# Kernel optimization log

Hardware: AMD Instinct MI355X
Metric: run time of the kernel (lower is better)

The kernel has to match this reference:

```python
import jax, jax.numpy as jnp
import numpy as np
from jax import lax

B, Hm, Wm, C, HEADS, MLP_H = 16, 56, 56, 256, 4, 1024
N = Hm * Wm
GRID_STRIDE = 4
N_GRID = (Hm // GRID_STRIDE) * (Wm // GRID_STRIDE)  # 196
K_DOWN = N // 4                                      # 784
K_ADA = K_DOWN - N_GRID
H2, W2 = Hm // 2, Wm // 2
POOL = 7


def _token_order():
    # get_loc: grid tokens first, then adaptive tokens
    pos = np.arange(N)
    tmp = pos.reshape(Hm, Wm)
    pos_grid = tmp[GRID_STRIDE // 2::GRID_STRIDE, GRID_STRIDE // 2::GRID_STRIDE].reshape(-1)
    m = np.ones(N, bool)
    m[pos_grid] = False
    return np.concatenate([pos_grid, pos[m]])


def _loc_init():
    y = 2.0 * ((np.arange(Hm) + 0.5) / Hm) - 1.0
    x = 2.0 * ((np.arange(Wm) + 0.5) / Wm) - 1.0
    xm, ym = np.meshgrid(x, y)
    return np.stack([xm, ym], -1).reshape(-1, 2).astype(np.float32)


_ORDER = _token_order()
_LOC = _loc_init()[_ORDER]


def _ln(x, g, b, eps=1e-5):
    m = jnp.mean(x, -1, keepdims=True)
    v = jnp.mean((x - m) ** 2, -1, keepdims=True)
    return (x - m) * lax.rsqrt(v + eps) * g + b


def _gauss_kernel(ks=3, sigma=2.0):
    c = np.arange(ks, dtype=np.float32)
    xg = np.tile(c, ks).reshape(ks, ks)
    yg = xg.T
    mean = (ks - 1) / 2.0
    var = sigma ** 2
    k = np.exp(-((xg - mean) ** 2 + (yg - mean) ** 2) / (2 * var)) / (2 * np.pi * var)
    return (k / k.sum()).astype(np.float32)


def _gauss_filt(x):
    ch = x.shape[1]
    w = jnp.broadcast_to(jnp.asarray(_gauss_kernel())[None, None], (ch, 1, 3, 3))
    return lax.conv_general_dilated(x, w, (1, 1), [(1, 1), (1, 1)],
                                    feature_group_count=ch,
                                    dimension_numbers=('NCHW', 'OIHW', 'NCHW'))


def _token2map(x, loc, H, W):
    # scatter-add tokens into a [H,W] map, average by count, gaussian hole-fill
    b, n, c = x.shape
    loc = jnp.clip(loc, -1, 1)
    px = jnp.clip(jnp.round(0.5 * (loc[..., 0] + 1) * W - 0.5).astype(jnp.int32), 0, W - 1)
    py = jnp.clip(jnp.round(0.5 * (loc[..., 1] + 1) * H - 0.5).astype(jnp.int32), 0, H - 1)
    idx = (px + py * W + jnp.arange(b)[:, None] * H * W).reshape(-1)
    src = jnp.concatenate([x, jnp.ones((b, n, 1), x.dtype)], -1).reshape(b * n, c + 1)
    out = jnp.zeros((b * H * W, c + 1), x.dtype).at[idx].add(src)
    out = out.reshape(b, H, W, c + 1).transpose(0, 3, 1, 2)
    feat, mask = out[:, :c], out[:, c:]
    feat = feat / (mask + 1e-6)
    mask = (mask > 0).astype(x.dtype)
    feat = feat * mask
    # reconstruct_feature (kernel_size=3, sigma=2)
    fm = _gauss_filt(jnp.concatenate([feat, mask], 1))
    fi = fm[:, :c] / (fm[:, c:] + 1e-6)
    mi = (fm[:, c:] > 0).astype(x.dtype)
    fi = fi * mi
    return feat + (1 - mask) * fi


def _map2token(fm, loc):
    # bilinear grid_sample, align_corners=False, zeros padding
    b, c, H, W = fm.shape
    x = (loc[..., 0] + 1) * 0.5 * W - 0.5
    y = (loc[..., 1] + 1) * 0.5 * H - 0.5
    x0 = jnp.floor(x)
    y0 = jnp.floor(y)
    wx = x - x0
    wy = y - y0
    fm_flat = fm.reshape(b, c, H * W)

    def gather(xi, yi):
        valid = ((xi >= 0) & (xi < W) & (yi >= 0) & (yi < H)).astype(fm.dtype)
        ii = (jnp.clip(yi, 0, H - 1) * W + jnp.clip(xi, 0, W - 1)).astype(jnp.int32)
        v = jnp.take_along_axis(fm_flat, ii[:, None, :], axis=2)  # [b,c,k]
        return v * valid[:, None, :]

    x0i = x0.astype(jnp.int32)
    y0i = y0.astype(jnp.int32)
    v00 = gather(x0i, y0i)
    v01 = gather(x0i + 1, y0i)
    v10 = gather(x0i, y0i + 1)
    v11 = gather(x0i + 1, y0i + 1)
    wx = wx[:, None, :]
    wy = wy[:, None, :]
    out = (v00 * (1 - wx) * (1 - wy) + v01 * wx * (1 - wy)
           + v10 * (1 - wx) * wy + v11 * wx * wy)
    return out.transpose(0, 2, 1)  # [b,k,c]


def _forward(x, ln1_g, ln1_b, wq, wkv, wproj, bproj, sr_w, sr_b, srn_g, srn_b,
             ln2_g, ln2_b, fc1_w, fc1_b, dw_w, dw_b, fc2_w, fc2_b, conf_w, conf_b):
    order = jnp.asarray(_ORDER)
    x = jnp.take(x, order, axis=1)                       # get_loc reorder
    loc = jnp.broadcast_to(jnp.asarray(_LOC)[None], (B, N, 2))
    d = C // HEADS
    # ---- PVT attention (spatial-reduction via 7x7 adaptive pool + 1x1 conv)
    xn = _ln(x, ln1_g, ln1_b)
    q = (xn @ wq).reshape(B, N, HEADS, d).transpose(0, 2, 1, 3)
    fmap = xn.transpose(0, 2, 1).reshape(B, C, Hm, Wm)
    pooled = fmap.reshape(B, C, POOL, Hm // POOL, POOL, Wm // POOL).mean((3, 5))
    sr = jnp.einsum('bihw,oi->bohw', pooled, sr_w) + sr_b[None, :, None, None]
    t = sr.reshape(B, C, POOL * POOL).transpose(0, 2, 1)
    t = jax.nn.gelu(_ln(t, srn_g, srn_b), approximate=False)
    kv = (t @ wkv).reshape(B, POOL * POOL, 2, HEADS, d)
    k = kv[:, :, 0].transpose(0, 2, 1, 3)
    v = kv[:, :, 1].transpose(0, 2, 1, 3)
    a = jax.nn.softmax(jnp.einsum('bhnd,bhmd->bhnm', q, k) * (d ** -0.5), axis=-1)
    o = jnp.einsum('bhnm,bhmd->bhnd', a, v).transpose(0, 2, 1, 3).reshape(B, N, C)
    x = x + o @ wproj + bproj
    # ---- MLP with depthwise conv
    xn = _ln(x, ln2_g, ln2_b)
    h = jax.nn.relu(xn @ fc1_w + fc1_b)
    hm = h.transpose(0, 2, 1).reshape(B, MLP_H, Hm, Wm)
    hm = lax.conv_general_dilated(hm, dw_w, (1, 1), [(1, 1), (1, 1)],
                                  feature_group_count=MLP_H,
                                  dimension_numbers=('NCHW', 'OIHW', 'NCHW'))
    hm = hm + dw_b[None, :, None, None]
    h = jax.nn.gelu(hm.reshape(B, MLP_H, N).transpose(0, 2, 1), approximate=False)
    x = x + h @ fc2_w + fc2_b
    # ---- gumbel top-k selection among adaptive tokens (grid tokens kept)
    conf = (x @ conf_w + conf_b)[..., 0]                 # [B,N]
    u = jax.random.uniform(jax.random.key(1), (B, N - N_GRID), x.dtype)
    g = -jnp.log(-jnp.log(u + 1e-6) + 1e-6)
    scores = conf[:, N_GRID:] + g                        # T=1
    _, idx = lax.top_k(scores, K_ADA)
    x_ada = jnp.take_along_axis(x[:, N_GRID:], idx[..., None], axis=1)
    loc_ada = jnp.take_along_axis(loc[:, N_GRID:], idx[..., None], axis=1)
    x_down = jnp.concatenate([x[:, :N_GRID], x_ada], 1)      # [B,784,C]
    loc_down = jnp.concatenate([loc[:, :N_GRID], loc_ada], 1)
    # ---- token2map (scatter-add + gaussian fill) then map2token (grid sample)
    fmap2 = _token2map(x, loc, H2, W2)
    tok = _map2token(fmap2, loc_down)
    return x_down + tok


def setup_inputs() -> dict:
    key = jax.random.key(0)
    ks = jax.random.split(key, 10)
    s = 0.02

    def rn(k, shape):
        return jax.random.normal(k, shape, jnp.float32) * s

    return {
        'x': jax.random.normal(ks[0], (B, N, C), jnp.float32),
        'ln1_g': jnp.ones((C,), jnp.float32), 'ln1_b': jnp.zeros((C,), jnp.float32),
        'wq': rn(ks[1], (C, C)), 'wkv': rn(ks[2], (C, 2 * C)),
        'wproj': rn(ks[3], (C, C)), 'bproj': jnp.zeros((C,), jnp.float32),
        'sr_w': rn(ks[4], (C, C)), 'sr_b': jnp.zeros((C,), jnp.float32),
        'srn_g': jnp.ones((C,), jnp.float32), 'srn_b': jnp.zeros((C,), jnp.float32),
        'ln2_g': jnp.ones((C,), jnp.float32), 'ln2_b': jnp.zeros((C,), jnp.float32),
        'fc1_w': rn(ks[5], (C, MLP_H)), 'fc1_b': jnp.zeros((MLP_H,), jnp.float32),
        'dw_w': rn(ks[6], (MLP_H, 1, 3, 3)), 'dw_b': jnp.zeros((MLP_H,), jnp.float32),
        'fc2_w': rn(ks[7], (MLP_H, C)), 'fc2_b': jnp.zeros((C,), jnp.float32),
        'conf_w': rn(ks[8], (C, 1)), 'conf_b': jnp.zeros((1,), jnp.float32),
    }


def reference(x, ln1_g, ln1_b, wq, wkv, wproj, bproj, sr_w, sr_b, srn_g, srn_b,
              ln2_g, ln2_b, fc1_w, fc1_b, dw_w, dw_b, fc2_w, fc2_b, conf_w, conf_b):
    return _forward(x, ln1_g, ln1_b, wq, wkv, wproj, bproj, sr_w, sr_b, srn_g, srn_b,
                    ln2_g, ln2_b, fc1_w, fc1_b, dw_w, dw_b, fc2_w, fc2_b, conf_w, conf_b)
```

## Files before the change

kernel.cpp:

```cpp
#include <hip/hip_runtime.h>
#include <math.h>


#define BB 16
#define NN 3136
#define CC 256
#define NHEADS 4
#define DH 64
#define MLPH 1024
#define NGRID 196
#define NREST 2940
#define KADA 588
#define HW 56
#define BCH 2

__device__ __forceinline__ int inv_order(int p) {
  int r = p / HW, c = p % HW;
  if ((r & 3) == 2 && (c & 3) == 2) return (r >> 2) * 14 + (c >> 2);
  int g = ((r + 1) >> 2) * 14 + (((r & 3) == 2) ? ((c + 1) >> 2) : 0);
  return NGRID + p - g;
}

__device__ __forceinline__ double gelu_d(double v) {
  return 0.5 * v * (1.0 + erf(v * 0.70710678118654752440));
}

__device__ __forceinline__ void tf2x32k(unsigned k0, unsigned k1, unsigned x0, unsigned x1,
                                        unsigned& o0, unsigned& o1) {
  unsigned ks[3] = {k0, k1, k0 ^ k1 ^ 0x1BD11BDAu};
  x0 += ks[0]; x1 += ks[1];
  const int rot[2][4] = {{13,15,26,6},{17,29,16,24}};
  #pragma unroll
  for (int i = 0; i < 5; ++i) {
    #pragma unroll
    for (int j = 0; j < 4; ++j) {
      int rr = rot[i & 1][j];
      x0 += x1;
      x1 = (x1 << rr) | (x1 >> (32 - rr));
      x1 ^= x0;
    }
    x0 += ks[(i + 1) % 3];
    x1 += ks[(i + 2) % 3] + (unsigned)(i + 1);
  }
  o0 = x0; o1 = x1;
}

__device__ bool tf_kat() {
  unsigned a, b;
  tf2x32k(0u, 0u, 0u, 0u, a, b);
  if (a != 0x6b200159u || b != 0x99ba4efeu) return false;
  tf2x32k(0xffffffffu, 0xffffffffu, 0xffffffffu, 0xffffffffu, a, b);
  if (a != 0x1cb996fcu || b != 0xbb002be7u) return false;
  tf2x32k(0x13198a2eu, 0x03707344u, 0x243f6a88u, 0x85a308d3u, a, b);
  if (a != 0xc4923a9cu || b != 0x483df7a0u) return false;
  return true;
}

__device__ __forceinline__ double gumbel_d(int f) {
  unsigned o0, o1;
  tf2x32k(0u, 1u, 0u, (unsigned)f, o0, o1);
  unsigned bits = o0 ^ o1;
  float u = __uint_as_float((bits >> 9) | 0x3f800000u) - 1.0f;
  double ud = (double)u;
  return -log(-log(ud + 1e-6) + 1e-6);
}

__global__ void k_order(int* __restrict__ ord) {
  int p = blockIdx.x * 256 + threadIdx.x;
  if (p < NN) ord[inv_order(p)] = p;
}

__global__ __launch_bounds__(256) void k_ln1(const float* __restrict__ x,
    const float* __restrict__ g, const float* __restrict__ b2,
    float* __restrict__ x_r, float* __restrict__ xn) {
  int b = blockIdx.x / NN, p = blockIdx.x % NN;
  int t = threadIdx.x;
  __shared__ double la[4], lb[4];
  float v = x[((size_t)b*NN + p)*CC + t];
  double vd = (double)v;
  double s = vd;
  #pragma unroll
  for (int o = 32; o; o >>= 1) s += __shfl_xor(s, o, 64);
  if ((t & 63) == 0) la[t >> 6] = s;
  __syncthreads();
  double m = (la[0] + la[1] + la[2] + la[3]) * (1.0/CC);
  double d = vd - m;
  s = d * d;
  #pragma unroll
  for (int o = 32; o; o >>= 1) s += __shfl_xor(s, o, 64);
  if ((t & 63) == 0) lb[t >> 6] = s;
  __syncthreads();
  double var = (lb[0] + lb[1] + lb[2] + lb[3]) * (1.0/CC);
  double o2 = d * (1.0 / sqrt(var + 1e-5)) * (double)g[t] + (double)b2[t];
  int n = inv_order(p);
  size_t dst = ((size_t)b*NN + n)*CC + t;
  x_r[dst] = v;
  xn[dst] = (float)o2;
}

__global__ __launch_bounds__(256) void k_ln2(const float* __restrict__ xin,
    const float* __restrict__ g, const float* __restrict__ b2, float* __restrict__ xo) {
  int row = blockIdx.x;
  int t = threadIdx.x;
  __shared__ double la[4], lb[4];
  double v = (double)xin[(size_t)row*CC + t];
  double s = v;
  #pragma unroll
  for (int o = 32; o; o >>= 1) s += __shfl_xor(s, o, 64);
  if ((t & 63) == 0) la[t >> 6] = s;
  __syncthreads();
  double m = (la[0] + la[1] + la[2] + la[3]) * (1.0/CC);
  double d = v - m;
  s = d * d;
  #pragma unroll
  for (int o = 32; o; o >>= 1) s += __shfl_xor(s, o, 64);
  if ((t & 63) == 0) lb[t >> 6] = s;
  __syncthreads();
  double var = (lb[0] + lb[1] + lb[2] + lb[3]) * (1.0/CC);
  xo[(size_t)row*CC + t] = (float)(d * (1.0 / sqrt(var + 1e-5)) * (double)g[t] + (double)b2[t]);
}

__global__ __launch_bounds__(256) void k_sr(const float* __restrict__ xn,
    const float* __restrict__ sr_w, const float* __restrict__ sr_b, float* __restrict__ srout) {
  int b = blockIdx.x / 49, cell = blockIdx.x % 49;
  int p1 = cell / 7, p2 = cell % 7;
  int t = threadIdx.x;
  __shared__ double pl[256];
  double s = 0.0;
  #pragma unroll
  for (int i = 0; i < 8; ++i)
    #pragma unroll
    for (int j = 0; j < 8; ++j) {
      int n = (p1*8 + i)*HW + (p2*8 + j);
      s += (double)xn[((size_t)b*NN + n)*CC + t];
    }
  pl[t] = s * (1.0/64.0);
  __syncthreads();
  double acc = (double)sr_b[t];
  for (int i = 0; i < CC; ++i) acc += pl[i] * (double)sr_w[t*CC + i];
  srout[((size_t)b*49 + cell)*CC + t] = (float)acc;
}

__global__ __launch_bounds__(256) void k_kv(const float* __restrict__ srout,
    const float* __restrict__ g, const float* __restrict__ b2,
    const float* __restrict__ wkv, float* __restrict__ kb, float* __restrict__ vb) {
  int b = blockIdx.x / 49, m = blockIdx.x % 49;
  int t = threadIdx.x;
  __shared__ double la[4], lb[4];
  __shared__ double tl[256];
  double v = (double)srout[((size_t)b*49 + m)*CC + t];
  double s = v;
  #pragma unroll
  for (int o = 32; o; o >>= 1) s += __shfl_xor(s, o, 64);
  if ((t & 63) == 0) la[t >> 6] = s;
  __syncthreads();
  double mean = (la[0] + la[1] + la[2] + la[3]) * (1.0/CC);
  double d = v - mean;
  s = d * d;
  #pragma unroll
  for (int o = 32; o; o >>= 1) s += __shfl_xor(s, o, 64);
  if ((t & 63) == 0) lb[t >> 6] = s;
  __syncthreads();
  double var = (lb[0] + lb[1] + lb[2] + lb[3]) * (1.0/CC);
  double o2 = d * (1.0 / sqrt(var + 1e-5)) * (double)g[t] + (double)b2[t];
  tl[t] = gelu_d(o2);
  __syncthreads();
  #pragma unroll
  for (int rep = 0; rep < 2; ++rep) {
    int j = t + rep*256;
    double acc = 0.0;
    for (int i = 0; i < CC; ++i) acc += tl[i] * (double)wkv[(size_t)i*512 + j];
    int h = (j >> 6) & 3, dd = j & 63;
    float* dst = (j >> 8) ? vb : kb;
    dst[(((size_t)b*NHEADS + h)*49 + m)*DH + dd] = (float)acc;
  }
}

template<int BIAS, int RELU, int RESID>
__global__ __launch_bounds__(256, 2) void k_gemmC(const float* __restrict__ A,
    const float* __restrict__ Bw, const float* __restrict__ bias,
    const float* resid, float* Co, int M, int N, int K) {
  __shared__ __align__(16) float As[16][132];
  __shared__ __align__(16) float Bs[16][132];
  int tid = threadIdx.x;
  int n0 = blockIdx.x * 128, m0 = blockIdx.y * 128;
  int tx = tid & 15, ty = tid >> 4;
  int aM = tid >> 1, aK = (tid & 1) * 8;
  int bK = tid >> 4, bN = (tid & 15) * 8;
  double acc[8][8] = {};
  for (int k0 = 0; k0 < K; k0 += 16) {
    const float* Ap = A + (size_t)(m0 + aM) * K + k0 + aK;
    float4 a0 = *(const float4*)Ap;
    float4 a1 = *(const float4*)(Ap + 4);
    As[aK+0][aM] = a0.x; As[aK+1][aM] = a0.y; As[aK+2][aM] = a0.z; As[aK+3][aM] = a0.w;
    As[aK+4][aM] = a1.x; As[aK+5][aM] = a1.y; As[aK+6][aM] = a1.z; As[aK+7][aM] = a1.w;
    const float* Bp = Bw + (size_t)(k0 + bK) * N + n0 + bN;
    *(float4*)&Bs[bK][bN]     = *(const float4*)Bp;
    *(float4*)&Bs[bK][bN + 4] = *(const float4*)(Bp + 4);
    __syncthreads();
    #pragma unroll
    for (int k = 0; k < 16; ++k) {
      double av[8], bv[8];
      #pragma unroll
      for (int r = 0; r < 8; ++r) av[r] = (double)As[k][ty*8 + r];
      #pragma unroll
      for (int c = 0; c < 8; ++c) bv[c] = (double)Bs[k][tx*8 + c];
      #pragma unroll
      for (int r = 0; r < 8; ++r)
        #pragma unroll
        for (int c = 0; c < 8; ++c)
          acc[r][c] = fma(av[r], bv[c], acc[r][c]);
    }
    __syncthreads();
  }
  #pragma unroll
  for (int r = 0; r < 8; ++r) {
    size_t off = (size_t)(m0 + ty*8 + r) * N + n0 + tx*8;
    #pragma unroll
    for (int c = 0; c < 8; ++c) {
      double v = acc[r][c];
      if (BIAS)  v += (double)bias[n0 + tx*8 + c];
      if (RESID) v += (double)resid[off + c];
      if (RELU)  v = fmax(v, 0.0);
      Co[off + c] = (float)v;
    }
  }
}

template<int BIAS, int RELU, int RESID>
__global__ __launch_bounds__(256) void k_gemmA(const float* __restrict__ A,
    const float* __restrict__ Bw, const float* __restrict__ bias,
    const float* resid, float* Co, int M, int N, int K) {
  __shared__ __align__(16) float As[16][132];
  __shared__ __align__(16) float Bs[16][68];
  int tid = threadIdx.x;
  int n0 = blockIdx.x * 64, m0 = blockIdx.y * 128;
  int tx = tid & 15, ty = tid >> 4;
  int aM = tid >> 2, aK = (tid & 3) * 4;
  int bK = tid >> 4, bN = (tid & 15) * 4;
  double acc[8][4] = {};
  for (int k0 = 0; k0 < K; k0 += 16) {
    #pragma unroll
    for (int ps = 0; ps < 2; ++ps) {
      float4 a4 = *(const float4*)&A[(size_t)(m0 + aM + ps*64) * K + k0 + aK];
      As[aK+0][aM+ps*64] = a4.x; As[aK+1][aM+ps*64] = a4.y;
      As[aK+2][aM+ps*64] = a4.z; As[aK+3][aM+ps*64] = a4.w;
    }
    float4 b4 = *(const float4*)&Bw[(size_t)(k0 + bK) * N + n0 + bN];
    *(float4*)&Bs[bK][bN] = b4;
    __syncthreads();
    #pragma unroll
    for (int k = 0; k < 16; ++k) {
      double av[8], bv[4];
      #pragma unroll
      for (int r = 0; r < 8; ++r) av[r] = (double)As[k][ty*8 + r];
      #pragma unroll
      for (int c = 0; c < 4; ++c) bv[c] = (double)Bs[k][tx*4 + c];
      #pragma unroll
      for (int r = 0; r < 8; ++r)
        #pragma unroll
        for (int c = 0; c < 4; ++c)
          acc[r][c] = fma(av[r], bv[c], acc[r][c]);
    }
    __syncthreads();
  }
  #pragma unroll
  for (int r = 0; r < 8; ++r) {
    size_t off = (size_t)(m0 + ty*8 + r) * N + n0 + tx*4;
    #pragma unroll
    for (int c = 0; c < 4; ++c) {
      double v = acc[r][c];
      if (BIAS)  v += (double)bias[n0 + tx*4 + c];
      if (RESID) v += (double)resid[off + c];
      if (RELU)  v = fmax(v, 0.0);
      Co[off + c] = (float)v;
    }
  }
}

__global__ __launch_bounds__(256) void k_attn(float* __restrict__ q,
    const float* __restrict__ kb, const float* __restrict__ vb) {
  int bh = blockIdx.x / 49, tile = blockIdx.x % 49;
  int b = bh >> 2, h = bh & 3;
  int tid = threadIdx.x;
  int w = tid >> 6, lane = tid & 63;
  __shared__ float Kt[64][53];
  __shared__ float Vs[49][64];
  __shared__ float qsw[4][64];
  __shared__ double Ps[4][52];
  const size_t kvbase = ((size_t)bh * 49) * DH;
  for (int idx = tid; idx < 49*64; idx += 256) {
    int m = idx >> 6, d = idx & 63;
    Kt[d][m] = kb[kvbase + idx];
    ((float*)Vs)[idx] = vb[kvbase + idx];
  }
  __syncthreads();
  #pragma unroll 1
  for (int t16 = 0; t16 < 16; ++t16) {
    int tok = tile*64 + w*16 + t16;
    size_t qoff = ((size_t)b*NN + tok)*CC + h*64 + lane;
    qsw[w][lane] = q[qoff];
    double lg = -1e300;
    if (lane < 49) {
      double acc = 0.0;
      #pragma unroll 16
      for (int d = 0; d < 64; ++d)
        acc = fma((double)qsw[w][d], (double)Kt[d][lane], acc);
      lg = acc * 0.125;
    }
    double mx = lg;
    #pragma unroll
    for (int o = 32; o; o >>= 1) mx = fmax(mx, __shfl_xor(mx, o, 64));
    double e = (lane < 49) ? exp(lg - mx) : 0.0;
    double s = e;
    #pragma unroll
    for (int o = 32; o; o >>= 1) s += __shfl_xor(s, o, 64);
    double sinv = 1.0 / s;
    if (lane < 49) Ps[w][lane] = e;
    double acc = 0.0;
    #pragma unroll 7
    for (int m = 0; m < 49; ++m)
      acc = fma(Ps[w][m], (double)Vs[m][lane], acc);
    q[qoff] = (float)(acc * sinv);
  }
}

__global__ __launch_bounds__(256) void k_dw(const float* __restrict__ hb,
    const float* __restrict__ w, const float* __restrict__ bias, float* __restrict__ h2) {
  int bl = blockIdx.x / NN, n = blockIdx.x % NN;
  int r = n / HW, c = n % HW;
  int t = threadIdx.x;
  const size_t base = (size_t)bl * NN;
  #pragma unroll
  for (int it = 0; it < 4; ++it) {
    int mc = t + it*256;
    double acc = (double)bias[mc];
    #pragma unroll
    for (int ky = 0; ky < 3; ++ky) {
      int rr = r + ky - 1;
      if (rr < 0 || rr >= HW) continue;
      #pragma unroll
      for (int kx = 0; kx < 3; ++kx) {
        int cc2 = c + kx - 1;
        if (cc2 < 0 || cc2 >= HW) continue;
        acc = fma((double)w[mc*9 + ky*3 + kx], (double)hb[(base + rr*HW + cc2)*MLPH + mc], acc);
      }
    }
    h2[(base + n)*MLPH + mc] = (float)gelu_d(acc);
  }
}

__global__ __launch_bounds__(256) void k_conf(const float* __restrict__ x3,
    const float* __restrict__ cw, const float* __restrict__ cb, double* __restrict__ scd) {
  int wid = (blockIdx.x * 256 + threadIdx.x) >> 6;
  int lane = threadIdx.x & 63;
  if (wid >= BB * NREST) return;
  int b = wid / NREST, i = wid % NREST;
  const float* xr = x3 + ((size_t)b*NN + NGRID + i)*CC;
  double acc = 0.0;
  #pragma unroll
  for (int r = 0; r < 4; ++r)
    acc += (double)xr[lane + r*64] * (double)cw[lane + r*64];
  #pragma unroll
  for (int o = 32; o; o >>= 1) acc += __shfl_xor(acc, o, 64);
  if (lane == 0) scd[wid] = acc + (double)cb[0] + gumbel_d(wid);
}

__global__ __launch_bounds__(512) void k_topk2(const double* __restrict__ scd, int* __restrict__ sel) {
  int b = blockIdx.x / 6, chunk = blockIdx.x % 6;
  __shared__ double sc[NREST];
  const double* s = scd + (size_t)b * NREST;
  for (int j = threadIdx.x; j < NREST; j += 512) sc[j] = s[j];
  __syncthreads();
  int i = chunk * 512 + threadIdx.x;
  if (i < NREST) {
    double si = sc[i];
    int rank = 0;
    #pragma unroll 8
    for (int j = 0; j < NREST; ++j) {
      double sj = sc[j];
      rank += (int)((sj > si) | ((sj == si) & (j < i)));
    }
    if (rank < KADA) sel[b*KADA + rank] = NGRID + i;
  }
}

__global__ __launch_bounds__(256) void k_t2m(const float* __restrict__ x3, float* __restrict__ fm) {
  int b = blockIdx.x / 784, pix = blockIdx.x % 784;
  int py = pix / 28, px = pix % 28;
  int t = threadIdx.x;
  float s = 0.f;
  #pragma unroll
  for (int dy = 0; dy < 2; ++dy)
    #pragma unroll
    for (int dx = 0; dx < 2; ++dx) {
      int p = (2*py + dy)*HW + 2*px + dx;
      s += x3[((size_t)b*NN + inv_order(p))*CC + t];
    }
  fm[((size_t)b*784 + pix)*CC + t] = s * (1.0f / 4.000001f);
}

__global__ __launch_bounds__(256) void k_out(const float* __restrict__ x3,
    const float* __restrict__ fm, const int* __restrict__ sel,
    const int* __restrict__ ord, float* __restrict__ out) {
  int b = blockIdx.x / 784, slot = blockIdx.x % 784;
  int t = threadIdx.x;
  int n = (slot < NGRID) ? slot : sel[b*KADA + slot - NGRID];
  int p = ord[n];
  int r = p / HW, c = p % HW;
  int ix0 = (c - 1) >> 1;
  int iy0 = (r - 1) >> 1;
  float wx = (c & 1) ? 0.25f : 0.75f;
  float wy = (r & 1) ? 0.25f : 0.75f;
  const float* fb = fm + (size_t)b*784*CC + t;
  float v = 0.f;
  float w00 = (1.f-wx)*(1.f-wy), w01 = wx*(1.f-wy), w10 = (1.f-wx)*wy, w11 = wx*wy;
  if (ix0 >= 0   && iy0 >= 0)   v += w00 * fb[(iy0*28 + ix0)*CC];
  if (ix0+1 < 28 && iy0 >= 0)   v += w01 * fb[(iy0*28 + ix0+1)*CC];
  if (ix0 >= 0   && iy0+1 < 28) v += w10 * fb[((iy0+1)*28 + ix0)*CC];
  if (ix0+1 < 28 && iy0+1 < 28) v += w11 * fb[((iy0+1)*28 + ix0+1)*CC];
  float res = x3[((size_t)b*NN + n)*CC + t] + v;
  if (blockIdx.x == 0 && t == 0) {
    if (!tf_kat()) res += 1000.0f;
  }
  out[((size_t)b*784 + slot)*CC + t] = res;
}

extern "C" void kernel_launch(void* const* d_in, const int* in_sizes, int n_in,
                              void* d_out, int out_size, void* d_ws, size_t ws_size,
                              hipStream_t stream) {
  const float* x      = (const float*)d_in[0];
  const float* ln1_g  = (const float*)d_in[1];
  const float* ln1_b  = (const float*)d_in[2];
  const float* wq     = (const float*)d_in[3];
  const float* wkv    = (const float*)d_in[4];
  const float* wproj  = (const float*)d_in[5];
  const float* bproj  = (const float*)d_in[6];
  const float* sr_w   = (const float*)d_in[7];
  const float* sr_b   = (const float*)d_in[8];
  const float* srn_g  = (const float*)d_in[9];
  const float* srn_b  = (const float*)d_in[10];
  const float* ln2_g  = (const float*)d_in[11];
  const float* ln2_b  = (const float*)d_in[12];
  const float* fc1_w  = (const float*)d_in[13];
  const float* fc1_b  = (const float*)d_in[14];
  const float* dw_w   = (const float*)d_in[15];
  const float* dw_b   = (const float*)d_in[16];
  const float* fc2_w  = (const float*)d_in[17];
  const float* fc2_b  = (const float*)d_in[18];
  const float* conf_w = (const float*)d_in[19];
  const float* conf_b = (const float*)d_in[20];
  float* out = (float*)d_out;

  float* ws = (float*)d_ws;
  const size_t SZ_XN = (size_t)BB*NN*CC;
  const size_t SZ_H  = (size_t)BCH*NN*MLPH;
  float* x_r   = ws;
  float* xn    = x_r + SZ_XN;
  float* qbuf  = xn + SZ_XN;
  float* hb    = qbuf + SZ_XN;
  float* h2b   = hb + SZ_H;
  float* srout = h2b + SZ_H;
  float* kb    = srout + (size_t)BB*49*CC;
  float* vb    = kb + (size_t)BB*NHEADS*49*DH;
  float* fm    = vb + (size_t)BB*NHEADS*49*DH;
  double* scd  = (double*)(fm + (size_t)BB*784*CC);
  int*   sel   = (int*)(scd + (size_t)BB*NREST);
  int*   ord   = sel + BB*KADA;

  k_order<<<(NN+255)/256, 256, 0, stream>>>(ord);
  k_ln1<<<BB*NN, 256, 0, stream>>>(x, ln1_g, ln1_b, x_r, xn);
  k_sr<<<BB*49, 256, 0, stream>>>(xn, sr_w, sr_b, srout);
  k_kv<<<BB*49, 256, 0, stream>>>(srout, srn_g, srn_b, wkv, kb, vb);
  k_gemmC<0,0,0><<<dim3(CC/128, BB*NN/128), 256, 0, stream>>>(xn, wq, nullptr, nullptr, qbuf, BB*NN, CC, CC);
  k_attn<<<BB*NHEADS*49, 256, 0, stream>>>(qbuf, kb, vb);
  k_gemmC<1,0,1><<<dim3(CC/128, BB*NN/128), 256, 0, stream>>>(qbuf, wproj, bproj, x_r, x_r, BB*NN, CC, CC);
  k_ln2<<<BB*NN, 256, 0, stream>>>(x_r, ln2_g, ln2_b, xn);
  for (int bc = 0; bc < BB/BCH; ++bc) {
    const size_t ro = (size_t)bc * BCH * NN;
    k_gemmC<1,1,0><<<dim3(MLPH/128, BCH*NN/128), 256, 0, stream>>>(xn + ro*CC, fc1_w, fc1_b, nullptr, hb, BCH*NN, MLPH, CC);
    k_dw<<<BCH*NN, 256, 0, stream>>>(hb, dw_w, dw_b, h2b);
    k_gemmA<1,0,1><<<dim3(CC/64, BCH*NN/128), 256, 0, stream>>>(h2b, fc2_w, fc2_b, x_r + ro*CC, x_r + ro*CC, BCH*NN, CC, MLPH);
  }
  k_conf<<<(BB*NREST*64 + 255)/256, 256, 0, stream>>>(x_r, conf_w, conf_b, scd);
  k_topk2<<<BB*6, 512, 0, stream>>>(scd, sel);
  k_t2m<<<BB*784, 256, 0, stream>>>(x_r, fm);
  k_out<<<BB*784, 256, 0, stream>>>(x_r, fm, sel, ord, out);
}
```

Measured before the change: 3.733 ms.

## Use FP64 MFMA matrix instructions for all dense GEMMs with runtime layout probe

Replaces the scalar double-precision FMA GEMM kernels (gemmC and gemmA) with one kernel built on the 16x16x4 f64 MFMA instruction. Each wave computes a 64x64 sub-tile. A tiny probe kernel runs first and finds the operand and output lane layout at runtime, and the GEMM reads that layout to index its operands and write back. The aim is to move the FP64 matrix work from vector ALUs to matrix cores; the cost is an extra launch, runtime-indexed addressing, and scattered epilogue stores. The fc2 GEMM now uses 128-wide N tiles, halving its block count.

```diff
diff --git a/kernel.cpp b/kernel.cpp
--- a/kernel.cpp
+++ b/kernel.cpp
@@ -14,6 +14,8 @@
 #define HW 56
 #define BCH 2
 
+typedef double v4d __attribute__((ext_vector_type(4)));
+
 __device__ __forceinline__ int inv_order(int p) {
   int r = p / HW, c = p % HW;
   if ((r & 3) == 2 && (c & 3) == 2) return (r >> 2) * 14 + (c >> 2);
@@ -65,6 +67,42 @@
   return -log(-log(ud + 1e-6) + 1e-6);
 }
 
+__global__ __launch_bounds__(64) void k_probe(int* __restrict__ combo) {
+  int l = threadIdx.x;
+  __shared__ double Am[16][4];
+  __shared__ double Bm[4][16];
+  __shared__ int found;
+  if (l == 0) found = -1;
+  {
+    int i = l >> 2, k = l & 3;
+    Am[i][k] = (double)((i*7 + k*3) % 13) - 6.0;
+    int k2 = l >> 4, j = l & 15;
+    Bm[k2][j] = (double)((k2*5 + j*11) % 17) - 8.0;
+  }
+  __syncthreads();
+  for (int c = 0; c < 16; ++c) {
+    int asw = c & 1, bsw = (c >> 1) & 1, dtr = (c >> 2) & 1, din = (c >> 3) & 1;
+    double a = Am[asw ? (l >> 2) : (l & 15)][asw ? (l & 3) : (l >> 4)];
+    double b = Bm[bsw ? (l & 3) : (l >> 4)][bsw ? (l >> 2) : (l & 15)];
+    v4d d = (v4d){0.0, 0.0, 0.0, 0.0};
+    d = __builtin_amdgcn_mfma_f64_16x16x4f64(a, b, d, 0, 0, 0);
+    int ok = 1;
+    #pragma unroll
+    for (int r = 0; r < 4; ++r) {
+      int rl = din ? ((l >> 4) + 4*r) : ((l >> 4)*4 + r);
+      int cl = l & 15;
+      int row = dtr ? cl : rl, col = dtr ? rl : cl;
+      double ref = 0.0;
+      #pragma unroll
+      for (int k = 0; k < 4; ++k) ref += Am[row][k] * Bm[k][col];
+      ok &= (d[r] == ref) ? 1 : 0;
+    }
+    if (__all(ok) && l == 0 && found < 0) found = c;
+  }
+  __syncthreads();
+  if (l == 0) combo[0] = found;
+}
+
 __global__ void k_order(int* __restrict__ ord) {
   int p = blockIdx.x * 256 + threadIdx.x;
   if (p < NN) ord[inv_order(p)] = p;
@@ -177,17 +215,30 @@
 }
 
 template<int BIAS, int RELU, int RESID>
-__global__ __launch_bounds__(256, 2) void k_gemmC(const float* __restrict__ A,
+__global__ __launch_bounds__(256) void k_gemmM(const float* __restrict__ A,
     const float* __restrict__ Bw, const float* __restrict__ bias,
-    const float* resid, float* Co, int M, int N, int K) {
-  __shared__ __align__(16) float As[16][132];
-  __shared__ __align__(16) float Bs[16][132];
+    const float* resid, float* Co, int M, int N, int K,
+    const int* __restrict__ combo) {
+  __shared__ float As[16][136];
+  __shared__ float Bs[16][136];
+  int cc = combo[0];
+  int asw = cc & 1, bsw = (cc >> 1) & 1, dtr = (cc >> 2) & 1, din = (cc >> 3) & 1;
   int tid = threadIdx.x;
   int n0 = blockIdx.x * 128, m0 = blockIdx.y * 128;
-  int tx = tid & 15, ty = tid >> 4;
+  int w = tid >> 6, lane = tid & 63;
+  int wr = w >> 1, wc = w & 1;
+  int raA = asw ? (lane >> 2) : (lane & 15);
+  int kaA = asw ? (lane & 3)  : (lane >> 4);
+  int rbB = bsw ? (lane >> 2) : (lane & 15);
+  int kbB = bsw ? (lane & 3)  : (lane >> 4);
   int aM = tid >> 1, aK = (tid & 1) * 8;
   int bK = tid >> 4, bN = (tid & 15) * 8;
-  double acc[8][8] = {};
+  v4d acc[4][4];
+  #pragma unroll
+  for (int m = 0; m < 4; ++m)
+    #pragma unroll
+    for (int n = 0; n < 4; ++n)
+      acc[m][n] = (v4d){0.0, 0.0, 0.0, 0.0};
   for (int k0 = 0; k0 < K; k0 += 16) {
     const float* Ap = A + (size_t)(m0 + aM) * K + k0 + aK;
     float4 a0 = *(const float4*)Ap;
@@ -199,81 +250,39 @@
     *(float4*)&Bs[bK][bN + 4] = *(const float4*)(Bp + 4);
     __syncthreads();
     #pragma unroll
-    for (int k = 0; k < 16; ++k) {
-      double av[8], bv[8];
+    for (int kk = 0; kk < 4; ++kk) {
+      double af[4], bf[4];
       #pragma unroll
-      for (int r = 0; r < 8; ++r) av[r] = (double)As[k][ty*8 + r];
+      for (int m = 0; m < 4; ++m) af[m] = (double)As[kk*4 + kaA][wr*64 + m*16 + raA];
       #pragma unroll
-      for (int c = 0; c < 8; ++c) bv[c] = (double)Bs[k][tx*8 + c];
+      for (int n = 0; n < 4; ++n) bf[n] = (double)Bs[kk*4 + kbB][wc*64 + n*16 + rbB];
       #pragma unroll
-      for (int r = 0; r < 8; ++r)
+      for (int m = 0; m < 4; ++m)
         #pragma unroll
-        for (int c = 0; c < 8; ++c)
-          acc[r][c] = fma(av[r], bv[c], acc[r][c]);
+        for (int n = 0; n < 4; ++n)
+          acc[m][n] = __builtin_amdgcn_mfma_f64_16x16x4f64(af[m], bf[n], acc[m][n], 0, 0, 0);
     }
     __syncthreads();
   }
-  #pragma unroll
-  for (int r = 0; r < 8; ++r) {
-    size_t off = (size_t)(m0 + ty*8 + r) * N + n0 + tx*8;
-    #pragma unroll
-    for (int c = 0; c < 8; ++c) {
-      double v = acc[r][c];
-      if (BIAS)  v += (double)bias[n0 + tx*8 + c];
-      if (RESID) v += (double)resid[off + c];
-      if (RELU)  v = fmax(v, 0.0);
-      Co[off + c] = (float)v;
-    }
-  }
-}
-
-template<int BIAS, int RELU, int RESID>
-__global__ __launch_bounds__(256) void k_gemmA(const float* __restrict__ A,
-    const float* __restrict__ Bw, const float* __restrict__ bias,
-    const float* resid, float* Co, int M, int N, int K) {
-  __shared__ __align__(16) float As[16][132];
-  __shared__ __align__(16) float Bs[16][68];
-  int tid = threadIdx.x;
-  int n0 = blockIdx.x * 64, m0 = blockIdx.y * 128;
-  int tx = tid & 15, ty = tid >> 4;
-  int aM = tid >> 2, aK = (tid & 3) * 4;
-  int bK = tid >> 4, bN = (tid & 15) * 4;
-  double acc[8][4] = {};
-  for (int k0 = 0; k0 < K; k0 += 16) {
-    #pragma unroll
-    for (int ps = 0; ps < 2; ++ps) {
-      float4 a4 = *(const float4*)&A[(size_t)(m0 + aM + ps*64) * K + k0 + aK];
-      As[aK+0][aM+ps*64] = a4.x; As[aK+1][aM+ps*64] = a4.y;
-      As[aK+2][aM+ps*64] = a4.z; As[aK+3][aM+ps*64] = a4.w;
-    }
-    float4 b4 = *(const float4*)&Bw[(size_t)(k0 + bK) * N + n0 + bN];
-    *(float4*)&Bs[bK][bN] = b4;
-    __syncthreads();
-    #pragma unroll
-    for (int k = 0; k < 16; ++k) {
-      double av[8], bv[4];
+  int lk = lane >> 4, lr = lane & 15;
+  #pragma unroll
+  for (int m = 0; m < 4; ++m) {
+    #pragma unroll
+    for (int n = 0; n < 4; ++n) {
       #pragma unroll
-      for (int r = 0; r < 8; ++r) av[r] = (double)As[k][ty*8 + r];
-      #pragma unroll
-      for (int c = 0; c < 4; ++c) bv[c] = (double)Bs[k][tx*4 + c];
-      #pragma unroll
-      for (int r = 0; r < 8; ++r)
-        #pragma unroll
-        for (int c = 0; c < 4; ++c)
-          acc[r][c] = fma(av[r], bv[c], acc[r][c]);
-    }
-    __syncthreads();
-  }
-  #pragma unroll
-  for (int r = 0; r < 8; ++r) {
-    size_t off = (size_t)(m0 + ty*8 + r) * N + n0 + tx*4;
-    #pragma unroll
-    for (int c = 0; c < 4; ++c) {
-      double v = acc[r][c];
-      if (BIAS)  v += (double)bias[n0 + tx*4 + c];
-      if (RESID) v += (double)resid[off + c];
-      if (RELU)  v = fmax(v, 0.0);
-      Co[off + c] = (float)v;
+      for (int r = 0; r < 4; ++r) {
+        int rl = din ? (lk + 4*r) : (lk*4 + r);
+        int rloc = dtr ? lr : rl;
+        int cloc = dtr ? rl : lr;
+        int row = m0 + wr*64 + m*16 + rloc;
+        int col = n0 + wc*64 + n*16 + cloc;
+        size_t off = (size_t)row * N + col;
+        double v = acc[m][n][r];
+        if (BIAS)  v += (double)bias[col];
+        if (RESID) v += (double)resid[off];
+        if (RELU)  v = fmax(v, 0.0);
+        Co[off] = (float)v;
+      }
     }
   }
 }
@@ -402,7 +411,8 @@
 
 __global__ __launch_bounds__(256) void k_out(const float* __restrict__ x3,
     const float* __restrict__ fm, const int* __restrict__ sel,
-    const int* __restrict__ ord, float* __restrict__ out) {
+    const int* __restrict__ ord, const int* __restrict__ combo,
+    float* __restrict__ out) {
   int b = blockIdx.x / 784, slot = blockIdx.x % 784;
   int t = threadIdx.x;
   int n = (slot < NGRID) ? slot : sel[b*KADA + slot - NGRID];
@@ -422,6 +432,7 @@
   float res = x3[((size_t)b*NN + n)*CC + t] + v;
   if (blockIdx.x == 0 && t == 0) {
     if (!tf_kat()) res += 1000.0f;
+    if (combo[0] < 0) res += 2000.0f;
   }
   out[((size_t)b*784 + slot)*CC + t] = res;
 }
@@ -467,23 +478,25 @@
   double* scd  = (double*)(fm + (size_t)BB*784*CC);
   int*   sel   = (int*)(scd + (size_t)BB*NREST);
   int*   ord   = sel + BB*KADA;
-
+  int*   combo = ord + NN;
+
+  k_probe<<<1, 64, 0, stream>>>(combo);
   k_order<<<(NN+255)/256, 256, 0, stream>>>(ord);
   k_ln1<<<BB*NN, 256, 0, stream>>>(x, ln1_g, ln1_b, x_r, xn);
   k_sr<<<BB*49, 256, 0, stream>>>(xn, sr_w, sr_b, srout);
   k_kv<<<BB*49, 256, 0, stream>>>(srout, srn_g, srn_b, wkv, kb, vb);
-  k_gemmC<0,0,0><<<dim3(CC/128, BB*NN/128), 256, 0, stream>>>(xn, wq, nullptr, nullptr, qbuf, BB*NN, CC, CC);
+  k_gemmM<0,0,0><<<dim3(CC/128, BB*NN/128), 256, 0, stream>>>(xn, wq, nullptr, nullptr, qbuf, BB*NN, CC, CC, combo);
   k_attn<<<BB*NHEADS*49, 256, 0, stream>>>(qbuf, kb, vb);
-  k_gemmC<1,0,1><<<dim3(CC/128, BB*NN/128), 256, 0, stream>>>(qbuf, wproj, bproj, x_r, x_r, BB*NN, CC, CC);
+  k_gemmM<1,0,1><<<dim3(CC/128, BB*NN/128), 256, 0, stream>>>(qbuf, wproj, bproj, x_r, x_r, BB*NN, CC, CC, combo);
   k_ln2<<<BB*NN, 256, 0, stream>>>(x_r, ln2_g, ln2_b, xn);
   for (int bc = 0; bc < BB/BCH; ++bc) {
     const size_t ro = (size_t)bc * BCH * NN;
-    k_gemmC<1,1,0><<<dim3(MLPH/128, BCH*NN/128), 256, 0, stream>>>(xn + ro*CC, fc1_w, fc1_b, nullptr, hb, BCH*NN, MLPH, CC);
+    k_gemmM<1,1,0><<<dim3(MLPH/128, BCH*NN/128), 256, 0, stream>>>(xn + ro*CC, fc1_w, fc1_b, nullptr, hb, BCH*NN, MLPH, CC, combo);
     k_dw<<<BCH*NN, 256, 0, stream>>>(hb, dw_w, dw_b, h2b);
-    k_gemmA<1,0,1><<<dim3(CC/64, BCH*NN/128), 256, 0, stream>>>(h2b, fc2_w, fc2_b, x_r + ro*CC, x_r + ro*CC, BCH*NN, CC, MLPH);
+    k_gemmM<1,0,1><<<dim3(CC/128, BCH*NN/128), 256, 0, stream>>>(h2b, fc2_w, fc2_b, x_r + ro*CC, x_r + ro*CC, BCH*NN, CC, MLPH, combo);
   }
   k_conf<<<(BB*NREST*64 + 255)/256, 256, 0, stream>>>(x_r, conf_w, conf_b, scd);
   k_topk2<<<BB*6, 512, 0, stream>>>(scd, sel);
   k_t2m<<<BB*784, 256, 0, stream>>>(x_r, fm);
-  k_out<<<BB*784, 256, 0, stream>>>(x_r, fm, sel, ord, out);
-}
+  k_out<<<BB*784, 256, 0, stream>>>(x_r, fm, sel, ord, combo, out);
+}
```

Result: slower. 4.000 ms (+7.1%).
